# Optimization experiments

Measured on AMD Instinct MI355X. Metric: run time of the kernel, lower is better.

Reference implementation:

```python
import jax, jax.numpy as jnp
import numpy as np


def setup_inputs() -> dict:
    key = jax.random.key(0)
    k1, k2, k3 = jax.random.split(key, 3)
    x = jax.random.normal(k1, (8, 3, 256, 256), dtype=jnp.float32)
    conv_w = jax.random.normal(k2, (64, 3), dtype=jnp.float32)  # 1x1 conv weight [O, C]
    w = jax.random.normal(k3, (64, 8), dtype=jnp.float32)       # per-channel LBP weights
    return {"x": x, "conv_w": conv_w, "w": w}


def _heaviside(d):
    # torch.heaviside(d, 0.): 1 where d > 0, else 0 (including d == 0)
    return jnp.where(d > 0, jnp.ones((), d.dtype), jnp.zeros((), d.dtype))


def reference(x, conv_w, w):
    # 1x1 conv, no bias: [N,C,H,W] x [O,C] -> [N,O,H,W]
    y = jnp.einsum('nchw,oc->nohw', x, conv_w)
    c = y[:, :, 1:-1, 1:-1]  # center, [N,O,H-2,W-2]
    # 8 neighbor shifts in the original order
    shifts = [
        y[:, :, 0:-2, 0:-2], y[:, :, 0:-2, 1:-1], y[:, :, 0:-2, 2:],
        y[:, :, 1:-1, 0:-2], y[:, :, 2:, 0:-2], y[:, :, 2:, 1:-1],
        y[:, :, 2:, 2:],    y[:, :, 1:-1, 2:],
    ]
    act = jnp.stack([_heaviside(c - s) for s in shifts], axis=2)  # [N,O,8,H-2,W-2]
    # weighted reduction over the 8 directions with exp(w)
    x_cat = jnp.einsum('nolhw,ol->nohw', act, jnp.exp(w))
    padded = jnp.pad(x_cat, ((0, 0), (0, 0), (1, 1), (1, 1)))  # ZeroPad2d(1)
    # res=True: concat raw input along channels -> [N, 3+O, H, W]
    return jnp.concatenate([x, padded], axis=1)
```

## Files before the change

kernel.cpp:

```cpp
#include <hip/hip_runtime.h>


__global__ __launch_bounds__(256) void lbp_all(
    const float* __restrict__ x,
    const float* __restrict__ conv_w,
    const float* __restrict__ w,
    float* __restrict__ out)
{
#pragma clang fp contract(off)
    const int n    = blockIdx.z;
    const int og   = blockIdx.y;
    const int h0   = blockIdx.x * 4;
    const int tid  = threadIdx.x;
    const int lane = tid & 63;
    const int wv   = tid >> 6;
    const int col  = lane * 4;

    __shared__ float xs[6][3][256];
    __shared__ float ys[6][256];
    __shared__ float ews[64];

    if (tid < 64) ews[tid] = expf(w[og * 64 + tid]);

    const float* xn = x + (size_t)n * 3 * 256 * 256;

    #pragma unroll
    for (int p = 0; p < 5; ++p) {
        const int u = wv + 4 * p;
        if (u < 18) {
            const int r  = u / 3;
            const int ch = u % 3;
            int row = h0 - 1 + r;
            row = row < 0 ? 0 : (row > 255 ? 255 : row);
            const float4 v = *(const float4*)(xn + ((ch * 256 + row) * 256 + col));
            *(float4*)&xs[r][ch][col] = v;
            if (og == 0 && r >= 1 && r <= 4) {
                *(float4*)(out + ((((size_t)n * 67 + ch) * 256 + (h0 + r - 1)) * 256 + col)) = v;
            }
        }
    }
    __syncthreads();

    for (int oi = 0; oi < 8; ++oi) {
        const int o = og * 8 + oi;
        const float cw0 = conv_w[o * 3 + 0];
        const float cw1 = conv_w[o * 3 + 1];
        const float cw2 = conv_w[o * 3 + 2];

        #pragma unroll
        for (int p = 0; p < 2; ++p) {
            const int r = wv + 4 * p;
            if (r < 6) {
                const float4 a = *(const float4*)&xs[r][0][col];
                const float4 b = *(const float4*)&xs[r][1][col];
                const float4 c = *(const float4*)&xs[r][2][col];
                float4 yv;
                yv.x = a.x * cw0 + b.x * cw1 + c.x * cw2;
                yv.y = a.y * cw0 + b.y * cw1 + c.y * cw2;
                yv.z = a.z * cw0 + b.z * cw1 + c.z * cw2;
                yv.w = a.w * cw0 + b.w * cw1 + c.w * cw2;
                *(float4*)&ys[r][col] = yv;
            }
        }
        __syncthreads();

        float Y[3][6];
        #pragma unroll
        for (int r = 0; r < 3; ++r) {
            const float4 v = *(const float4*)&ys[wv + r][col];
            Y[r][1] = v.x; Y[r][2] = v.y; Y[r][3] = v.z; Y[r][4] = v.w;
            Y[r][0] = __shfl_up(v.w, 1);
            Y[r][5] = __shfl_down(v.x, 1);
        }

        const float e0 = ews[oi * 8 + 0], e1 = ews[oi * 8 + 1];
        const float e2 = ews[oi * 8 + 2], e3 = ews[oi * 8 + 3];
        const float e4 = ews[oi * 8 + 4], e5 = ews[oi * 8 + 5];
        const float e6 = ews[oi * 8 + 6], e7 = ews[oi * 8 + 7];

        const int hrow = h0 + wv;
        float res[4];
        if (hrow == 0 || hrow == 255) {
            res[0] = res[1] = res[2] = res[3] = 0.f;
        } else {
            #pragma unroll
            for (int j = 0; j < 4; ++j) {
                const int cidx = col + j;
                if ((cidx == 0) | (cidx == 255)) { res[j] = 0.f; continue; }
                const float c = Y[1][j + 1];
                float acc;
                acc  = (c > Y[0][j    ]) ? e0 : 0.f;
                acc += (c > Y[0][j + 1]) ? e1 : 0.f;
                acc += (c > Y[0][j + 2]) ? e2 : 0.f;
                acc += (c > Y[1][j    ]) ? e3 : 0.f;
                acc += (c > Y[2][j    ]) ? e4 : 0.f;
                acc += (c > Y[2][j + 1]) ? e5 : 0.f;
                acc += (c > Y[2][j + 2]) ? e6 : 0.f;
                acc += (c > Y[1][j + 2]) ? e7 : 0.f;
                res[j] = acc;
            }
        }
        *(float4*)(out + ((((size_t)n * 67 + 3 + o) * 256 + hrow) * 256 + col)) =
            make_float4(res[0], res[1], res[2], res[3]);

        __syncthreads();
    }
}

extern "C" void kernel_launch(void* const* d_in, const int* in_sizes, int n_in,
                              void* d_out, int out_size, void* d_ws, size_t ws_size,
                              hipStream_t stream) {
    const float* x      = (const float*)d_in[0];
    const float* conv_w = (const float*)d_in[1];
    const float* w      = (const float*)d_in[2];
    float* out          = (float*)d_out;

    dim3 grid(64, 8, 8);
    dim3 block(256);
    hipLaunchKernelGGL(lbp_all, grid, block, 0, stream, x, conv_w, w, out);
}
```

Measured before the change: 163.2 us.

## Keep input rows in registers, recompute conv per thread, drop LDS staging and barriers

Each thread now loads its three input rows (3 channels each) straight into registers and recomputes the 1x1 conv for its 3x4 neighbourhood, instead of staging x and y through shared memory with a barrier per output channel. Channels per block go from 8 to 16, which halves the grid and the redundant input loads. Boundary rows take an early exit that only writes zeros, and edge columns are zeroed by lane index. The cost is recomputing the conv three times per thread (overlapping rows across warps), higher register pressure, and fewer blocks to hide store latency.

```diff
diff --git a/kernel.cpp b/kernel.cpp
--- a/kernel.cpp
+++ b/kernel.cpp
@@ -15,62 +15,59 @@
     const int lane = tid & 63;
     const int wv   = tid >> 6;
     const int col  = lane * 4;
+    const int hrow = h0 + wv;
 
-    __shared__ float xs[6][3][256];
-    __shared__ float ys[6][256];
-    __shared__ float ews[64];
+    __shared__ float ews[128];
+    if (tid < 128) ews[tid] = expf(w[og * 128 + tid]);
 
-    if (tid < 64) ews[tid] = expf(w[og * 64 + tid]);
+    const float* xn = x + (size_t)n * 3 * 65536;
 
-    const float* xn = x + (size_t)n * 3 * 256 * 256;
+    float4 xr[3][3];
+    #pragma unroll
+    for (int r = 0; r < 3; ++r) {
+        int row = hrow - 1 + r;
+        row = row < 0 ? 0 : (row > 255 ? 255 : row);
+        #pragma unroll
+        for (int ch = 0; ch < 3; ++ch)
+            xr[r][ch] = *(const float4*)(xn + (ch * 256 + row) * 256 + col);
+    }
 
-    #pragma unroll
-    for (int p = 0; p < 5; ++p) {
-        const int u = wv + 4 * p;
-        if (u < 18) {
-            const int r  = u / 3;
-            const int ch = u % 3;
-            int row = h0 - 1 + r;
-            row = row < 0 ? 0 : (row > 255 ? 255 : row);
-            const float4 v = *(const float4*)(xn + ((ch * 256 + row) * 256 + col));
-            *(float4*)&xs[r][ch][col] = v;
-            if (og == 0 && r >= 1 && r <= 4) {
-                *(float4*)(out + ((((size_t)n * 67 + ch) * 256 + (h0 + r - 1)) * 256 + col)) = v;
-            }
-        }
+    if (og == 0) {
+        #pragma unroll
+        for (int ch = 0; ch < 3; ++ch)
+            *(float4*)(out + ((((size_t)n * 67 + ch) * 256 + hrow) * 256 + col)) = xr[1][ch];
     }
+
     __syncthreads();
 
-    for (int oi = 0; oi < 8; ++oi) {
-        const int o = og * 8 + oi;
+    float* obase = out + ((((size_t)n * 67 + 3 + og * 16) * 256 + hrow) * 256 + col);
+
+    if (hrow == 0 || hrow == 255) {
+        const float4 z = make_float4(0.f, 0.f, 0.f, 0.f);
+        #pragma unroll
+        for (int oi = 0; oi < 16; ++oi)
+            *(float4*)(obase + (size_t)oi * 65536) = z;
+        return;
+    }
+
+    #pragma unroll 2
+    for (int oi = 0; oi < 16; ++oi) {
+        const int o = og * 16 + oi;
         const float cw0 = conv_w[o * 3 + 0];
         const float cw1 = conv_w[o * 3 + 1];
         const float cw2 = conv_w[o * 3 + 2];
 
-        #pragma unroll
-        for (int p = 0; p < 2; ++p) {
-            const int r = wv + 4 * p;
-            if (r < 6) {
-                const float4 a = *(const float4*)&xs[r][0][col];
-                const float4 b = *(const float4*)&xs[r][1][col];
-                const float4 c = *(const float4*)&xs[r][2][col];
-                float4 yv;
-                yv.x = a.x * cw0 + b.x * cw1 + c.x * cw2;
-                yv.y = a.y * cw0 + b.y * cw1 + c.y * cw2;
-                yv.z = a.z * cw0 + b.z * cw1 + c.z * cw2;
-                yv.w = a.w * cw0 + b.w * cw1 + c.w * cw2;
-                *(float4*)&ys[r][col] = yv;
-            }
-        }
-        __syncthreads();
-
         float Y[3][6];
         #pragma unroll
         for (int r = 0; r < 3; ++r) {
-            const float4 v = *(const float4*)&ys[wv + r][col];
-            Y[r][1] = v.x; Y[r][2] = v.y; Y[r][3] = v.z; Y[r][4] = v.w;
-            Y[r][0] = __shfl_up(v.w, 1);
-            Y[r][5] = __shfl_down(v.x, 1);
+            float4 yv;
+            yv.x = xr[r][0].x * cw0 + xr[r][1].x * cw1 + xr[r][2].x * cw2;
+            yv.y = xr[r][0].y * cw0 + xr[r][1].y * cw1 + xr[r][2].y * cw2;
+            yv.z = xr[r][0].z * cw0 + xr[r][1].z * cw1 + xr[r][2].z * cw2;
+            yv.w = xr[r][0].w * cw0 + xr[r][1].w * cw1 + xr[r][2].w * cw2;
+            Y[r][1] = yv.x; Y[r][2] = yv.y; Y[r][3] = yv.z; Y[r][4] = yv.w;
+            Y[r][0] = __shfl_up(yv.w, 1);
+            Y[r][5] = __shfl_down(yv.x, 1);
         }
 
         const float e0 = ews[oi * 8 + 0], e1 = ews[oi * 8 + 1];
@@ -78,32 +75,26 @@
         const float e4 = ews[oi * 8 + 4], e5 = ews[oi * 8 + 5];
         const float e6 = ews[oi * 8 + 6], e7 = ews[oi * 8 + 7];
 
-        const int hrow = h0 + wv;
         float res[4];
-        if (hrow == 0 || hrow == 255) {
-            res[0] = res[1] = res[2] = res[3] = 0.f;
-        } else {
-            #pragma unroll
-            for (int j = 0; j < 4; ++j) {
-                const int cidx = col + j;
-                if ((cidx == 0) | (cidx == 255)) { res[j] = 0.f; continue; }
-                const float c = Y[1][j + 1];
-                float acc;
-                acc  = (c > Y[0][j    ]) ? e0 : 0.f;
-                acc += (c > Y[0][j + 1]) ? e1 : 0.f;
-                acc += (c > Y[0][j + 2]) ? e2 : 0.f;
-                acc += (c > Y[1][j    ]) ? e3 : 0.f;
-                acc += (c > Y[2][j    ]) ? e4 : 0.f;
-                acc += (c > Y[2][j + 1]) ? e5 : 0.f;
-                acc += (c > Y[2][j + 2]) ? e6 : 0.f;
-                acc += (c > Y[1][j + 2]) ? e7 : 0.f;
-                res[j] = acc;
-            }
+        #pragma unroll
+        for (int j = 0; j < 4; ++j) {
+            const float c = Y[1][j + 1];
+            float acc;
+            acc  = (c > Y[0][j    ]) ? e0 : 0.f;
+            acc += (c > Y[0][j + 1]) ? e1 : 0.f;
+            acc += (c > Y[0][j + 2]) ? e2 : 0.f;
+            acc += (c > Y[1][j    ]) ? e3 : 0.f;
+            acc += (c > Y[2][j    ]) ? e4 : 0.f;
+            acc += (c > Y[2][j + 1]) ? e5 : 0.f;
+            acc += (c > Y[2][j + 2]) ? e6 : 0.f;
+            acc += (c > Y[1][j + 2]) ? e7 : 0.f;
+            res[j] = acc;
         }
-        *(float4*)(out + ((((size_t)n * 67 + 3 + o) * 256 + hrow) * 256 + col)) =
+        if (lane == 0)  res[0] = 0.f;
+        if (lane == 63) res[3] = 0.f;
+
+        *(float4*)(obase + (size_t)oi * 65536) =
             make_float4(res[0], res[1], res[2], res[3]);
-
-        __syncthreads();
     }
 }
 
@@ -115,7 +106,7 @@
     const float* w      = (const float*)d_in[2];
     float* out          = (float*)d_out;
 
-    dim3 grid(64, 8, 8);
+    dim3 grid(64, 4, 8);
     dim3 block(256);
     hipLaunchKernelGGL(lbp_all, grid, block, 0, stream, x, conv_w, w, out);
 }
```

New measurement: 154.1 us. 1.06x faster.
